# Optimization experiments

Measured on AMD Instinct MI355X. Metric: run time of the kernel, lower is better.

The kernel has to match this reference:

```python
import jax, jax.numpy as jnp
import numpy as np

N = 50000   # n_nodes
E = 800000  # n_edges (directed)
D = 64      # feature dim (in = hidden = out = 64 per source)


def setup_inputs() -> dict:
    key = jax.random.key(0)
    ks = jax.random.split(key, 16)
    s = 0.1  # init scale
    inp = {
        "x": jax.random.normal(ks[0], (N, D), jnp.float32),
        "edge_index": jax.random.randint(ks[1], (2, E), 0, N),
        # GCNConv 1
        "W1": jax.random.normal(ks[2], (D, 64), jnp.float32) * s,
        "b1": jnp.zeros((64,), jnp.float32),
        # TransformerConv (heads=1): query/key/value + root (skip) linear
        "Wq": jax.random.normal(ks[3], (64, 64), jnp.float32) * s,
        "bq": jnp.zeros((64,), jnp.float32),
        "Wk": jax.random.normal(ks[4], (64, 64), jnp.float32) * s,
        "bk": jnp.zeros((64,), jnp.float32),
        "Wv": jax.random.normal(ks[5], (64, 64), jnp.float32) * s,
        "bv": jnp.zeros((64,), jnp.float32),
        "Ws": jax.random.normal(ks[6], (64, 64), jnp.float32) * s,
        "bs": jnp.zeros((64,), jnp.float32),
        # GCNConv 2
        "W2": jax.random.normal(ks[7], (64, D), jnp.float32) * s,
        "b2": jnp.zeros((D,), jnp.float32),
    }
    return inp


def gcn_conv(x, W, b, src, dst, n):
    """PyG GCNConv: symmetric normalization with self-loops, then scatter-add."""
    xw = x @ W  # [N, F]
    loop = jnp.arange(n)
    src2 = jnp.concatenate([src, loop])
    dst2 = jnp.concatenate([dst, loop])
    deg = jax.ops.segment_sum(jnp.ones(src2.shape[0], xw.dtype), dst2, num_segments=n)
    dinv = jnp.where(deg > 0, jax.lax.rsqrt(deg), 0.0)
    norm = dinv[src2] * dinv[dst2]  # [E+N]
    out = jax.ops.segment_sum(xw[src2] * norm[:, None], dst2, num_segments=n)
    return out + b


def segment_softmax(logits, seg, n):
    m = jax.ops.segment_max(logits, seg, num_segments=n)
    e = jnp.exp(logits - m[seg])
    z = jax.ops.segment_sum(e, seg, num_segments=n)
    return e / z[seg]


def transformer_conv(x, Wq, bq, Wk, bk, Wv, bv, Ws, bs, src, dst, n):
    """PyG TransformerConv (heads=1, concat=True, root_weight=True)."""
    q = x @ Wq + bq  # [N, 64]
    k = x @ Wk + bk
    v = x @ Wv + bv
    scale = jax.lax.rsqrt(jnp.asarray(q.shape[-1], q.dtype))
    logits = jnp.sum(q[dst] * k[src], axis=-1) * scale  # [E]
    alpha = segment_softmax(logits, dst, n)
    aggr = jax.ops.segment_sum(v[src] * alpha[:, None], dst, num_segments=n)
    return aggr + x @ Ws + bs  # root/skip connection


def reference(x, edge_index, W1, b1, Wq, bq, Wk, bk, Wv, bv, Ws, bs, W2, b2):
    src, dst = edge_index[0], edge_index[1]
    n = x.shape[0]
    x1 = jax.nn.relu(gcn_conv(x, W1, b1, src, dst, n))
    x2 = transformer_conv(x1, Wq, bq, Wk, bk, Wv, bv, Ws, bs, src, dst, n)
    x3 = gcn_conv(x2, W2, b2, src, dst, n)
    return x3
```

## Files before the change

kernel.cpp:

```cpp
#include <hip/hip_runtime.h>
#include <math.h>


#define D 64
#define BKT_SHIFT 9
#define CAP 12288
#define CHUNK 4096

__device__ __forceinline__ unsigned short f2bf(float f) {
    unsigned int u = __float_as_uint(f);
    u += 0x7FFFu + ((u >> 16) & 1u);
    return (unsigned short)(u >> 16);
}
#define BF_LO(u) __uint_as_float((u) << 16)
#define BF_HI(u) __uint_as_float((u) & 0xFFFF0000u)


__global__ void init_gcursor(int* __restrict__ gcursor) {
    if (threadIdx.x < 128) gcursor[threadIdx.x] = 0;
}

__global__ __launch_bounds__(256) void binA_kernel(const int* __restrict__ src,
                                                   const int* __restrict__ dst,
                                                   int* __restrict__ gcursor,
                                                   unsigned int* __restrict__ staging,
                                                   int e, int nbkt) {
    __shared__ int cntB[128];
    __shared__ int offB[128];
    __shared__ int curB[128];
    __shared__ int gbase[128];
    __shared__ unsigned int pairs[CHUNK];
    __shared__ unsigned char bkt[CHUNK];

    int t = threadIdx.x;
    int e0 = blockIdx.x * CHUNK;
    int ecnt = min(CHUNK, e - e0);

    if (t < 128) cntB[t] = 0;
    __syncthreads();

    int myS[CHUNK / 256], myD[CHUNK / 256];
    #pragma unroll
    for (int i = 0; i < CHUNK / 256; ++i) {
        int idx = t + 256 * i;
        if (idx < ecnt) {
            myS[i] = src[e0 + idx];
            myD[i] = dst[e0 + idx];
            atomicAdd(&cntB[myD[i] >> BKT_SHIFT], 1);
        }
    }
    __syncthreads();
    if (t < 128) offB[t] = cntB[t];
    __syncthreads();
    for (int off = 1; off < 128; off <<= 1) {
        int add = (t < 128 && t >= off) ? offB[t - off] : 0;
        __syncthreads();
        if (t < 128) offB[t] += add;
        __syncthreads();
    }
    if (t < 128) {
        int excl = offB[t] - cntB[t];
        offB[t] = excl;
        curB[t] = excl;
        if (t < nbkt && cntB[t] > 0) gbase[t] = atomicAdd(&gcursor[t], cntB[t]);
    }
    __syncthreads();
    #pragma unroll
    for (int i = 0; i < CHUNK / 256; ++i) {
        int idx = t + 256 * i;
        if (idx < ecnt) {
            int b = myD[i] >> BKT_SHIFT;
            int p = atomicAdd(&curB[b], 1);
            pairs[p] = ((unsigned int)myD[i] << 16) | (unsigned int)myS[i];
            bkt[p] = (unsigned char)b;
        }
    }
    __syncthreads();
    for (int p = t; p < ecnt; p += 256) {
        int b = bkt[p];
        staging[(size_t)b * CAP + gbase[b] + (p - offB[b])] = pairs[p];
    }
}

__global__ __launch_bounds__(256) void binB_kernel(const int* __restrict__ gcursor,
                                                   const unsigned int* __restrict__ staging,
                                                   unsigned short* __restrict__ esrc,
                                                   int* __restrict__ cnt,
                                                   int* __restrict__ rowptr,
                                                   float* __restrict__ dinv,
                                                   int n, int nbkt) {
    __shared__ int bpre[128];
    __shared__ int c512[512];
    __shared__ int o512[512];
    int t = threadIdx.x;
    int b = blockIdx.x;

    if (t < 128) bpre[t] = (t < nbkt) ? gcursor[t] : 0;
    __syncthreads();
    for (int off = 1; off < 128; off <<= 1) {
        int add = (t < 128 && t >= off) ? bpre[t - off] : 0;
        __syncthreads();
        if (t < 128) bpre[t] += add;
        __syncthreads();
    }
    int base_b = (b == 0) ? 0 : bpre[b - 1];
    int cnt_b = gcursor[b];
    int lo = b << BKT_SHIFT;

    c512[t] = 0; c512[t + 256] = 0;
    __syncthreads();
    const unsigned int* st = staging + (size_t)b * CAP;
    for (int i = t; i < cnt_b; i += 256)
        atomicAdd(&c512[(int)(st[i] >> 16) - lo], 1);
    __syncthreads();
    o512[t] = c512[t]; o512[t + 256] = c512[t + 256];
    __syncthreads();
    for (int off = 1; off < 512; off <<= 1) {
        int a1 = (t >= off) ? o512[t - off] : 0;
        int a2 = o512[t + 256 - off];
        __syncthreads();
        o512[t] += a1; o512[t + 256] += a2;
        __syncthreads();
    }
    int e1 = o512[t] - c512[t];
    int e2 = o512[t + 256] - c512[t + 256];
    __syncthreads();
    o512[t] = e1; o512[t + 256] = e2;
    __syncthreads();
    for (int i = t; i < 512; i += 256) {
        int g = lo + i;
        if (g < n) {
            int c = c512[i];
            cnt[g] = c;
            rowptr[g] = base_b + o512[i];
            dinv[g] = rsqrtf((float)c + 1.0f);
        }
    }
    __syncthreads();
    for (int i = t; i < cnt_b; i += 256) {
        unsigned int pk = st[i];
        int local = (int)(pk >> 16) - lo;
        int p = atomicAdd(&o512[local], 1);
        esrc[base_b + p] = (unsigned short)(pk & 0xFFFFu);
    }
}

__global__ __launch_bounds__(256) void gemm64_bf16s(const float* __restrict__ X,
                                                    const float* __restrict__ W,
                                                    const float* __restrict__ dinv,
                                                    unsigned short* __restrict__ xs, int n) {
    __shared__ float sX[64][68];
    __shared__ float sW[64 * 64];
    int t = threadIdx.x;
    int base = blockIdx.x * 64;
    #pragma unroll
    for (int i = 0; i < 4; ++i) {
        int f = t * 4 + i * 1024;
        *(float4*)&sW[f] = *(const float4*)&W[f];
        int r = f >> 6, c = f & 63;
        int row = base + r;
        float4 xv = (row < n) ? *(const float4*)&X[(size_t)row * D + c]
                              : make_float4(0.f, 0.f, 0.f, 0.f);
        *(float4*)&sX[r][c] = xv;
    }
    __syncthreads();

    int cg = t & 15, rg = t >> 4;
    int j0 = cg * 4, r0 = rg * 4;
    float acc[4][4];
    #pragma unroll
    for (int a = 0; a < 4; ++a)
        #pragma unroll
        for (int c = 0; c < 4; ++c) acc[a][c] = 0.0f;

    #pragma unroll 4
    for (int kk = 0; kk < 64; kk += 4) {
        float4 w0 = *(const float4*)&sW[(kk + 0) * 64 + j0];
        float4 w1 = *(const float4*)&sW[(kk + 1) * 64 + j0];
        float4 w2 = *(const float4*)&sW[(kk + 2) * 64 + j0];
        float4 w3 = *(const float4*)&sW[(kk + 3) * 64 + j0];
        #pragma unroll
        for (int a = 0; a < 4; ++a) {
            float4 xv = *(const float4*)&sX[r0 + a][kk];
            acc[a][0] = fmaf(xv.x, w0.x, acc[a][0]); acc[a][1] = fmaf(xv.x, w0.y, acc[a][1]);
            acc[a][2] = fmaf(xv.x, w0.z, acc[a][2]); acc[a][3] = fmaf(xv.x, w0.w, acc[a][3]);
            acc[a][0] = fmaf(xv.y, w1.x, acc[a][0]); acc[a][1] = fmaf(xv.y, w1.y, acc[a][1]);
            acc[a][2] = fmaf(xv.y, w1.z, acc[a][2]); acc[a][3] = fmaf(xv.y, w1.w, acc[a][3]);
            acc[a][0] = fmaf(xv.z, w2.x, acc[a][0]); acc[a][1] = fmaf(xv.z, w2.y, acc[a][1]);
            acc[a][2] = fmaf(xv.z, w2.z, acc[a][2]); acc[a][3] = fmaf(xv.z, w2.w, acc[a][3]);
            acc[a][0] = fmaf(xv.w, w3.x, acc[a][0]); acc[a][1] = fmaf(xv.w, w3.y, acc[a][1]);
            acc[a][2] = fmaf(xv.w, w3.z, acc[a][2]); acc[a][3] = fmaf(xv.w, w3.w, acc[a][3]);
        }
    }

    #pragma unroll
    for (int a = 0; a < 4; ++a) {
        int row = base + r0 + a;
        if (row < n) {
            float dv = dinv[row];
            ushort4 h;
            h.x = f2bf(acc[a][0] * dv);
            h.y = f2bf(acc[a][1] * dv);
            h.z = f2bf(acc[a][2] * dv);
            h.w = f2bf(acc[a][3] * dv);
            *(ushort4*)&xs[(size_t)row * D + j0] = h;
        }
    }
}

__global__ __launch_bounds__(512) void fusedA_kernel(const unsigned short* __restrict__ xs,
                                                     const float* __restrict__ dinv,
                                                     const int* __restrict__ rowptr,
                                                     const int* __restrict__ cnt,
                                                     const unsigned short* __restrict__ esrc,
                                                     const float* __restrict__ b1,
                                                     const float* __restrict__ Wq,
                                                     const float* __restrict__ bq,
                                                     const float* __restrict__ Wk,
                                                     const float* __restrict__ bk,
                                                     const float* __restrict__ Wv,
                                                     const float* __restrict__ bv,
                                                     const float* __restrict__ Ws,
                                                     const float* __restrict__ bs,
                                                     float* __restrict__ Yq,
                                                     unsigned short* __restrict__ kv,
                                                     float* __restrict__ Ysk, int n) {
    __shared__ float sX[64][68];
    __shared__ float sW[64 * 64];
    int t = threadIdx.x;
    int base = blockIdx.x * 64;
    int local = t >> 3, sub = t & 7;
    int j0 = sub * 8;
    int node = base + local;

    {
        float a[8] = {0.f, 0.f, 0.f, 0.f, 0.f, 0.f, 0.f, 0.f};
        float4 o0 = make_float4(0.f, 0.f, 0.f, 0.f);
        float4 o1 = make_float4(0.f, 0.f, 0.f, 0.f);
        if (node < n) {
            float dd = dinv[node];
            int start = rowptr[node], deg = cnt[node];
            uint4 sr = *(const uint4*)&xs[(size_t)node * D + j0];
            a[0] += BF_LO(sr.x); a[1] += BF_HI(sr.x);
            a[2] += BF_LO(sr.y); a[3] += BF_HI(sr.y);
            a[4] += BF_LO(sr.z); a[5] += BF_HI(sr.z);
            a[6] += BF_LO(sr.w); a[7] += BF_HI(sr.w);
            int i = 0;
            for (; i + 4 <= deg; i += 4) {
                int s0 = esrc[start + i + 0];
                int s1 = esrc[start + i + 1];
                int s2 = esrc[start + i + 2];
                int s3 = esrc[start + i + 3];
                uint4 r0 = *(const uint4*)&xs[(size_t)s0 * D + j0];
                uint4 r1 = *(const uint4*)&xs[(size_t)s1 * D + j0];
                uint4 r2 = *(const uint4*)&xs[(size_t)s2 * D + j0];
                uint4 r3 = *(const uint4*)&xs[(size_t)s3 * D + j0];
                a[0] += BF_LO(r0.x) + BF_LO(r1.x) + BF_LO(r2.x) + BF_LO(r3.x);
                a[1] += BF_HI(r0.x) + BF_HI(r1.x) + BF_HI(r2.x) + BF_HI(r3.x);
                a[2] += BF_LO(r0.y) + BF_LO(r1.y) + BF_LO(r2.y) + BF_LO(r3.y);
                a[3] += BF_HI(r0.y) + BF_HI(r1.y) + BF_HI(r2.y) + BF_HI(r3.y);
                a[4] += BF_LO(r0.z) + BF_LO(r1.z) + BF_LO(r2.z) + BF_LO(r3.z);
                a[5] += BF_HI(r0.z) + BF_HI(r1.z) + BF_HI(r2.z) + BF_HI(r3.z);
                a[6] += BF_LO(r0.w) + BF_LO(r1.w) + BF_LO(r2.w) + BF_LO(r3.w);
                a[7] += BF_HI(r0.w) + BF_HI(r1.w) + BF_HI(r2.w) + BF_HI(r3.w);
            }
            for (; i < deg; ++i) {
                int s = esrc[start + i];
                uint4 r = *(const uint4*)&xs[(size_t)s * D + j0];
                a[0] += BF_LO(r.x); a[1] += BF_HI(r.x);
                a[2] += BF_LO(r.y); a[3] += BF_HI(r.y);
                a[4] += BF_LO(r.z); a[5] += BF_HI(r.z);
                a[6] += BF_LO(r.w); a[7] += BF_HI(r.w);
            }
            float4 bb0 = *(const float4*)&b1[j0];
            float4 bb1 = *(const float4*)&b1[j0 + 4];
            o0.x = fmaxf(fmaf(dd, a[0], bb0.x), 0.f);
            o0.y = fmaxf(fmaf(dd, a[1], bb0.y), 0.f);
            o0.z = fmaxf(fmaf(dd, a[2], bb0.z), 0.f);
            o0.w = fmaxf(fmaf(dd, a[3], bb0.w), 0.f);
            o1.x = fmaxf(fmaf(dd, a[4], bb1.x), 0.f);
            o1.y = fmaxf(fmaf(dd, a[5], bb1.y), 0.f);
            o1.z = fmaxf(fmaf(dd, a[6], bb1.z), 0.f);
            o1.w = fmaxf(fmaf(dd, a[7], bb1.w), 0.f);
        }
        *(float4*)&sX[local][j0] = o0;
        *(float4*)&sX[local][j0 + 4] = o1;
    }

    int cg = t & 15, rg = t >> 4;
    int gj0 = cg * 4, r0 = rg * 2;

    #pragma unroll 1
    for (int w4 = 0; w4 < 4; ++w4) {
        const float* W = (w4 == 0) ? Wq : (w4 == 1) ? Wk : (w4 == 2) ? Wv : Ws;
        const float* B = (w4 == 0) ? bq : (w4 == 1) ? bk : (w4 == 2) ? bv : bs;
        __syncthreads();
        #pragma unroll
        for (int i = 0; i < 2; ++i) {
            int f = t * 4 + i * 2048;
            *(float4*)&sW[f] = *(const float4*)&W[f];
        }
        __syncthreads();

        float acc[2][4];
        #pragma unroll
        for (int a = 0; a < 2; ++a)
            #pragma unroll
            for (int c = 0; c < 4; ++c) acc[a][c] = 0.0f;

        #pragma unroll 4
        for (int kk = 0; kk < 64; kk += 4) {
            float4 w0 = *(const float4*)&sW[(kk + 0) * 64 + gj0];
            float4 w1 = *(const float4*)&sW[(kk + 1) * 64 + gj0];
            float4 w2 = *(const float4*)&sW[(kk + 2) * 64 + gj0];
            float4 w3 = *(const float4*)&sW[(kk + 3) * 64 + gj0];
            #pragma unroll
            for (int a = 0; a < 2; ++a) {
                float4 xv = *(const float4*)&sX[r0 + a][kk];
                acc[a][0] = fmaf(xv.x, w0.x, acc[a][0]); acc[a][1] = fmaf(xv.x, w0.y, acc[a][1]);
                acc[a][2] = fmaf(xv.x, w0.z, acc[a][2]); acc[a][3] = fmaf(xv.x, w0.w, acc[a][3]);
                acc[a][0] = fmaf(xv.y, w1.x, acc[a][0]); acc[a][1] = fmaf(xv.y, w1.y, acc[a][1]);
                acc[a][2] = fmaf(xv.y, w1.z, acc[a][2]); acc[a][3] = fmaf(xv.y, w1.w, acc[a][3]);
                acc[a][0] = fmaf(xv.z, w2.x, acc[a][0]); acc[a][1] = fmaf(xv.z, w2.y, acc[a][1]);
                acc[a][2] = fmaf(xv.z, w2.z, acc[a][2]); acc[a][3] = fmaf(xv.z, w2.w, acc[a][3]);
                acc[a][0] = fmaf(xv.w, w3.x, acc[a][0]); acc[a][1] = fmaf(xv.w, w3.y, acc[a][1]);
                acc[a][2] = fmaf(xv.w, w3.z, acc[a][2]); acc[a][3] = fmaf(xv.w, w3.w, acc[a][3]);
            }
        }

        float4 bb = *(const float4*)&B[gj0];
        if (w4 == 0) {
            #pragma unroll
            for (int a = 0; a < 2; ++a) {
                int row = base + r0 + a;
                if (row < n) {
                    float4 o = make_float4((acc[a][0] + bb.x) * 0.125f,
                                           (acc[a][1] + bb.y) * 0.125f,
                                           (acc[a][2] + bb.z) * 0.125f,
                                           (acc[a][3] + bb.w) * 0.125f);
                    *(float4*)&Yq[(size_t)row * D + gj0] = o;
                }
            }
        } else if (w4 == 3) {
            #pragma unroll
            for (int a = 0; a < 2; ++a) {
                int row = base + r0 + a;
                if (row < n) {
                    float4 o = make_float4(acc[a][0] + bb.x, acc[a][1] + bb.y,
                                           acc[a][2] + bb.z, acc[a][3] + bb.w);
                    *(float4*)&Ysk[(size_t)row * D + gj0] = o;
                }
            }
        } else {
            int off = (w4 == 1) ? 0 : 64;
            #pragma unroll
            for (int a = 0; a < 2; ++a) {
                int row = base + r0 + a;
                if (row < n) {
                    ushort4 h;
                    h.x = f2bf(acc[a][0] + bb.x);
                    h.y = f2bf(acc[a][1] + bb.y);
                    h.z = f2bf(acc[a][2] + bb.z);
                    h.w = f2bf(acc[a][3] + bb.w);
                    *(ushort4*)&kv[(size_t)row * 128 + off + gj0] = h;
                }
            }
        }
    }
}

__global__ __launch_bounds__(512) void fusedB_kernel(const float* __restrict__ q,
                                                     const unsigned short* __restrict__ kv,
                                                     const float* __restrict__ skip,
                                                     const float* __restrict__ dinv,
                                                     const int* __restrict__ rowptr,
                                                     const int* __restrict__ cnt,
                                                     const unsigned short* __restrict__ esrc,
                                                     const float* __restrict__ W2,
                                                     unsigned short* __restrict__ xs2, int n) {
    __shared__ float sX[64][68];
    __shared__ float sW[64 * 64];
    int t = threadIdx.x;
    int base = blockIdx.x * 64;
    int local = t >> 3, sub = t & 7;
    int j0 = sub * 8;
    int node = base + local;

    #pragma unroll
    for (int i = 0; i < 2; ++i) {
        int f = t * 4 + i * 2048;
        *(float4*)&sW[f] = *(const float4*)&W2[f];
    }

    {
        float4 o0 = make_float4(0.f, 0.f, 0.f, 0.f);
        float4 o1 = make_float4(0.f, 0.f, 0.f, 0.f);
        if (node < n) {
            int start = rowptr[node], deg = cnt[node];
            float4 q0 = *(const float4*)&q[(size_t)node * D + j0];
            float4 q1 = *(const float4*)&q[(size_t)node * D + j0 + 4];
            float4 s0 = *(const float4*)&skip[(size_t)node * D + j0];
            float4 s1 = *(const float4*)&skip[(size_t)node * D + j0 + 4];
            float z = 0.0f;
            float a[8] = {0.f, 0.f, 0.f, 0.f, 0.f, 0.f, 0.f, 0.f};
            int i = 0;
            for (; i + 4 <= deg; i += 4) {
                int e0 = esrc[start + i + 0];
                int e1 = esrc[start + i + 1];
                int e2 = esrc[start + i + 2];
                int e3 = esrc[start + i + 3];
                const unsigned short* r0p = kv + (size_t)e0 * 128;
                const unsigned short* r1p = kv + (size_t)e1 * 128;
                const unsigned short* r2p = kv + (size_t)e2 * 128;
                const unsigned short* r3p = kv + (size_t)e3 * 128;
                uint4 k0 = *(const uint4*)&r0p[j0];
                uint4 k1 = *(const uint4*)&r1p[j0];
                uint4 k2 = *(const uint4*)&r2p[j0];
                uint4 k3 = *(const uint4*)&r3p[j0];
                uint4 v0 = *(const uint4*)&r0p[64 + j0];
                uint4 v1 = *(const uint4*)&r1p[64 + j0];
                uint4 v2 = *(const uint4*)&r2p[64 + j0];
                uint4 v3 = *(const uint4*)&r3p[64 + j0];
                float p0 = q0.x * BF_LO(k0.x) + q0.y * BF_HI(k0.x)
                         + q0.z * BF_LO(k0.y) + q0.w * BF_HI(k0.y)
                         + q1.x * BF_LO(k0.z) + q1.y * BF_HI(k0.z)
                         + q1.z * BF_LO(k0.w) + q1.w * BF_HI(k0.w);
                float p1 = q0.x * BF_LO(k1.x) + q0.y * BF_HI(k1.x)
                         + q0.z * BF_LO(k1.y) + q0.w * BF_HI(k1.y)
                         + q1.x * BF_LO(k1.z) + q1.y * BF_HI(k1.z)
                         + q1.z * BF_LO(k1.w) + q1.w * BF_HI(k1.w);
                float p2 = q0.x * BF_LO(k2.x) + q0.y * BF_HI(k2.x)
                         + q0.z * BF_LO(k2.y) + q0.w * BF_HI(k2.y)
                         + q1.x * BF_LO(k2.z) + q1.y * BF_HI(k2.z)
                         + q1.z * BF_LO(k2.w) + q1.w * BF_HI(k2.w);
                float p3 = q0.x * BF_LO(k3.x) + q0.y * BF_HI(k3.x)
                         + q0.z * BF_LO(k3.y) + q0.w * BF_HI(k3.y)
                         + q1.x * BF_LO(k3.z) + q1.y * BF_HI(k3.z)
                         + q1.z * BF_LO(k3.w) + q1.w * BF_HI(k3.w);
                #pragma unroll
                for (int off = 1; off < 8; off <<= 1) {
                    p0 += __shfl_xor(p0, off, 64);
                    p1 += __shfl_xor(p1, off, 64);
                    p2 += __shfl_xor(p2, off, 64);
                    p3 += __shfl_xor(p3, off, 64);
                }
                float w0 = __expf(p0), w1 = __expf(p1), w2 = __expf(p2), w3 = __expf(p3);
                z += (w0 + w1) + (w2 + w3);
                a[0] += w0 * BF_LO(v0.x) + w1 * BF_LO(v1.x) + w2 * BF_LO(v2.x) + w3 * BF_LO(v3.x);
                a[1] += w0 * BF_HI(v0.x) + w1 * BF_HI(v1.x) + w2 * BF_HI(v2.x) + w3 * BF_HI(v3.x);
                a[2] += w0 * BF_LO(v0.y) + w1 * BF_LO(v1.y) + w2 * BF_LO(v2.y) + w3 * BF_LO(v3.y);
                a[3] += w0 * BF_HI(v0.y) + w1 * BF_HI(v1.y) + w2 * BF_HI(v2.y) + w3 * BF_HI(v3.y);
                a[4] += w0 * BF_LO(v0.z) + w1 * BF_LO(v1.z) + w2 * BF_LO(v2.z) + w3 * BF_LO(v3.z);
                a[5] += w0 * BF_HI(v0.z) + w1 * BF_HI(v1.z) + w2 * BF_HI(v2.z) + w3 * BF_HI(v3.z);
                a[6] += w0 * BF_LO(v0.w) + w1 * BF_LO(v1.w) + w2 * BF_LO(v2.w) + w3 * BF_LO(v3.w);
                a[7] += w0 * BF_HI(v0.w) + w1 * BF_HI(v1.w) + w2 * BF_HI(v2.w) + w3 * BF_HI(v3.w);
            }
            for (; i < deg; ++i) {
                int s = esrc[start + i];
                const unsigned short* row = kv + (size_t)s * 128;
                uint4 kr = *(const uint4*)&row[j0];
                uint4 vr = *(const uint4*)&row[64 + j0];
                float p = q0.x * BF_LO(kr.x) + q0.y * BF_HI(kr.x)
                        + q0.z * BF_LO(kr.y) + q0.w * BF_HI(kr.y)
                        + q1.x * BF_LO(kr.z) + q1.y * BF_HI(kr.z)
                        + q1.z * BF_LO(kr.w) + q1.w * BF_HI(kr.w);
                #pragma unroll
                for (int off = 1; off < 8; off <<= 1) p += __shfl_xor(p, off, 64);
                float w = __expf(p);
                z += w;
                a[0] += w * BF_LO(vr.x); a[1] += w * BF_HI(vr.x);
                a[2] += w * BF_LO(vr.y); a[3] += w * BF_HI(vr.y);
                a[4] += w * BF_LO(vr.z); a[5] += w * BF_HI(vr.z);
                a[6] += w * BF_LO(vr.w); a[7] += w * BF_HI(vr.w);
            }
            if (deg > 0) {
                float inv = 1.0f / z;
                o0.x = fmaf(a[0], inv, s0.x); o0.y = fmaf(a[1], inv, s0.y);
                o0.z = fmaf(a[2], inv, s0.z); o0.w = fmaf(a[3], inv, s0.w);
                o1.x = fmaf(a[4], inv, s1.x); o1.y = fmaf(a[5], inv, s1.y);
                o1.z = fmaf(a[6], inv, s1.z); o1.w = fmaf(a[7], inv, s1.w);
            } else {
                o0 = s0; o1 = s1;
            }
        }
        *(float4*)&sX[local][j0] = o0;
        *(float4*)&sX[local][j0 + 4] = o1;
    }
    __syncthreads();

    int cg = t & 15, rg = t >> 4;
    int gj0 = cg * 4, r0 = rg * 2;
    float acc[2][4];
    #pragma unroll
    for (int a = 0; a < 2; ++a)
        #pragma unroll
        for (int c = 0; c < 4; ++c) acc[a][c] = 0.0f;

    #pragma unroll 4
    for (int kk = 0; kk < 64; kk += 4) {
        float4 w0 = *(const float4*)&sW[(kk + 0) * 64 + gj0];
        float4 w1 = *(const float4*)&sW[(kk + 1) * 64 + gj0];
        float4 w2 = *(const float4*)&sW[(kk + 2) * 64 + gj0];
        float4 w3 = *(const float4*)&sW[(kk + 3) * 64 + gj0];
        #pragma unroll
        for (int a = 0; a < 2; ++a) {
            float4 xv = *(const float4*)&sX[r0 + a][kk];
            acc[a][0] = fmaf(xv.x, w0.x, acc[a][0]); acc[a][1] = fmaf(xv.x, w0.y, acc[a][1]);
            acc[a][2] = fmaf(xv.x, w0.z, acc[a][2]); acc[a][3] = fmaf(xv.x, w0.w, acc[a][3]);
            acc[a][0] = fmaf(xv.y, w1.x, acc[a][0]); acc[a][1] = fmaf(xv.y, w1.y, acc[a][1]);
            acc[a][2] = fmaf(xv.y, w1.z, acc[a][2]); acc[a][3] = fmaf(xv.y, w1.w, acc[a][3]);
            acc[a][0] = fmaf(xv.z, w2.x, acc[a][0]); acc[a][1] = fmaf(xv.z, w2.y, acc[a][1]);
            acc[a][2] = fmaf(xv.z, w2.z, acc[a][2]); acc[a][3] = fmaf(xv.z, w2.w, acc[a][3]);
            acc[a][0] = fmaf(xv.w, w3.x, acc[a][0]); acc[a][1] = fmaf(xv.w, w3.y, acc[a][1]);
            acc[a][2] = fmaf(xv.w, w3.z, acc[a][2]); acc[a][3] = fmaf(xv.w, w3.w, acc[a][3]);
        }
    }

    #pragma unroll
    for (int a = 0; a < 2; ++a) {
        int row = base + r0 + a;
        if (row < n) {
            float dv = dinv[row];
            ushort4 h;
            h.x = f2bf(acc[a][0] * dv);
            h.y = f2bf(acc[a][1] * dv);
            h.z = f2bf(acc[a][2] * dv);
            h.w = f2bf(acc[a][3] * dv);
            *(ushort4*)&xs2[(size_t)row * D + gj0] = h;
        }
    }
}

__global__ __launch_bounds__(256) void gcn_gather_kernel(const unsigned short* __restrict__ xs,
                                                         const float* __restrict__ dinv,
                                                         const int* __restrict__ rowptr,
                                                         const int* __restrict__ cnt,
                                                         const unsigned short* __restrict__ esrc,
                                                         const float* __restrict__ bias,
                                                         float* __restrict__ out,
                                                         int n, int relu) {
    int node = (blockIdx.x * blockDim.x + threadIdx.x) >> 6;
    if (node >= n) return;
    int lane = threadIdx.x & 63;
    int grp = lane >> 3;
    int sub = lane & 7;
    int j0 = sub * 8;

    int start = rowptr[node], deg = cnt[node];

    float a[8] = {0.f, 0.f, 0.f, 0.f, 0.f, 0.f, 0.f, 0.f};
    int i = grp;
    int sNext = (i < deg) ? esrc[start + i] : 0;
    for (; i < deg; i += 8) {
        int s = sNext;
        int in = i + 8;
        if (in < deg) sNext = esrc[start + in];
        uint4 r = *(const uint4*)&xs[(size_t)s * D + j0];
        a[0] += BF_LO(r.x); a[1] += BF_HI(r.x);
        a[2] += BF_LO(r.y); a[3] += BF_HI(r.y);
        a[4] += BF_LO(r.z); a[5] += BF_HI(r.z);
        a[6] += BF_LO(r.w); a[7] += BF_HI(r.w);
    }
    #pragma unroll
    for (int off = 8; off < 64; off <<= 1) {
        #pragma unroll
        for (int c = 0; c < 8; ++c) a[c] += __shfl_xor(a[c], off, 64);
    }

    if (grp == 0) {
        float dd = dinv[node];
        uint4 sr = *(const uint4*)&xs[(size_t)node * D + j0];
        a[0] += BF_LO(sr.x); a[1] += BF_HI(sr.x);
        a[2] += BF_LO(sr.y); a[3] += BF_HI(sr.y);
        a[4] += BF_LO(sr.z); a[5] += BF_HI(sr.z);
        a[6] += BF_LO(sr.w); a[7] += BF_HI(sr.w);
        float4 b0 = *(const float4*)&bias[j0];
        float4 b1 = *(const float4*)&bias[j0 + 4];
        float o[8];
        o[0] = fmaf(dd, a[0], b0.x); o[1] = fmaf(dd, a[1], b0.y);
        o[2] = fmaf(dd, a[2], b0.z); o[3] = fmaf(dd, a[3], b0.w);
        o[4] = fmaf(dd, a[4], b1.x); o[5] = fmaf(dd, a[5], b1.y);
        o[6] = fmaf(dd, a[6], b1.z); o[7] = fmaf(dd, a[7], b1.w);
        if (relu) {
            #pragma unroll
            for (int c = 0; c < 8; ++c) o[c] = fmaxf(o[c], 0.f);
        }
        *(float4*)&out[(size_t)node * D + j0] = make_float4(o[0], o[1], o[2], o[3]);
        *(float4*)&out[(size_t)node * D + j0 + 4] = make_float4(o[4], o[5], o[6], o[7]);
    }
}


extern "C" void kernel_launch(void* const* d_in, const int* in_sizes, int n_in,
                              void* d_out, int out_size, void* d_ws, size_t ws_size,
                              hipStream_t stream) {
    const float* x  = (const float*)d_in[0];
    const int*   ei = (const int*)d_in[1];
    const float* W1 = (const float*)d_in[2];
    const float* b1 = (const float*)d_in[3];
    const float* Wq = (const float*)d_in[4];
    const float* bq = (const float*)d_in[5];
    const float* Wk = (const float*)d_in[6];
    const float* bk = (const float*)d_in[7];
    const float* Wv = (const float*)d_in[8];
    const float* bv = (const float*)d_in[9];
    const float* Ws = (const float*)d_in[10];
    const float* bs = (const float*)d_in[11];
    const float* W2 = (const float*)d_in[12];
    const float* b2 = (const float*)d_in[13];
    float* out = (float*)d_out;

    const int n = in_sizes[0] / D;
    const int e = in_sizes[1] / 2;
    const int* src = ei;
    const int* dst = ei + e;
    const int n64 = n * D;
    const int nbkt = (n + (1 << BKT_SHIFT) - 1) >> BKT_SHIFT;

    char* w = (char*)d_ws;
    auto carve = [&](size_t bytes) {
        char* p = w;
        w += (bytes + 255) & ~(size_t)255;
        return p;
    };
    int* gcursor            = (int*)carve(128 * 4);
    unsigned int* staging   = (unsigned int*)carve((size_t)nbkt * CAP * 4);
    unsigned short* esrc    = (unsigned short*)carve((size_t)e * 2);
    int* cnt                = (int*)carve((size_t)n * 4);
    int* rowptr             = (int*)carve((size_t)n * 4);
    float* dinv             = (float*)carve((size_t)n * 4);
    float* bufQ             = (float*)carve((size_t)n64 * 4);
    unsigned short* xs      = (unsigned short*)carve((size_t)n64 * 2);
    unsigned short* kv      = (unsigned short*)carve((size_t)n64 * 4);

    const int nb_binA = (e + CHUNK - 1) / CHUNK;
    const int nb_nw   = (n + 3) / 4;
    const int nb_g    = (n + 63) / 64;

    init_gcursor<<<1, 128, 0, stream>>>(gcursor);
    binA_kernel<<<nb_binA, 256, 0, stream>>>(src, dst, gcursor, staging, e, nbkt);
    binB_kernel<<<nbkt, 256, 0, stream>>>(gcursor, staging, esrc, cnt, rowptr, dinv, n, nbkt);

    gemm64_bf16s<<<nb_g, 256, 0, stream>>>(x, W1, dinv, xs, n);

    fusedA_kernel<<<nb_g, 512, 0, stream>>>(xs, dinv, rowptr, cnt, esrc, b1,
                                            Wq, bq, Wk, bk, Wv, bv, Ws, bs,
                                            bufQ, kv, out, n);

    fusedB_kernel<<<nb_g, 512, 0, stream>>>(bufQ, kv, out, dinv,
                                            rowptr, cnt, esrc, W2, xs, n);

    gcn_gather_kernel<<<nb_nw, 256, 0, stream>>>(xs, dinv, rowptr, cnt, esrc,
                                                 b2, out, n, 0);
}
```

Before: 252.2 us.

## Sort nodes by in-degree and process them through a permutation for load balance

Result: slower. 509.6 us (+102.1%).

```diff
diff --git a/kernel.cpp b/kernel.cpp
--- a/kernel.cpp
+++ b/kernel.cpp
@@ -17,7 +17,7 @@
 
 
 __global__ void init_gcursor(int* __restrict__ gcursor) {
-    if (threadIdx.x < 128) gcursor[threadIdx.x] = 0;
+    if (threadIdx.x < 192) gcursor[threadIdx.x] = 0;
 }
 
 __global__ __launch_bounds__(256) void binA_kernel(const int* __restrict__ src,
@@ -88,6 +88,7 @@
                                                    int* __restrict__ cnt,
                                                    int* __restrict__ rowptr,
                                                    float* __restrict__ dinv,
+                                                   int* __restrict__ deghist,
                                                    int n, int nbkt) {
     __shared__ int bpre[128];
     __shared__ int c512[512];
@@ -134,6 +135,7 @@
             cnt[g] = c;
             rowptr[g] = base_b + o512[i];
             dinv[g] = rsqrtf((float)c + 1.0f);
+            atomicAdd(&deghist[63 - min(c, 63)], 1);
         }
     }
     __syncthreads();
@@ -142,6 +144,27 @@
         int local = (int)(pk >> 16) - lo;
         int p = atomicAdd(&o512[local], 1);
         esrc[base_b + p] = (unsigned short)(pk & 0xFFFFu);
+    }
+}
+
+__global__ void degscan_kernel(int* __restrict__ deghist) {
+    if (threadIdx.x == 0) {
+        int run = 0;
+        for (int i = 0; i < 64; ++i) {
+            int c = deghist[i];
+            deghist[i] = run;
+            run += c;
+        }
+    }
+}
+
+__global__ void degscatter_kernel(const int* __restrict__ cnt, int* __restrict__ degbase,
+                                  int* __restrict__ perm, int n) {
+    int i = blockIdx.x * blockDim.x + threadIdx.x;
+    if (i < n) {
+        int bin = 63 - min(cnt[i], 63);
+        int pos = atomicAdd(&degbase[bin], 1);
+        perm[pos] = i;
     }
 }
 
@@ -213,6 +236,7 @@
                                                      const int* __restrict__ rowptr,
                                                      const int* __restrict__ cnt,
                                                      const unsigned short* __restrict__ esrc,
+                                                     const int* __restrict__ perm,
                                                      const float* __restrict__ b1,
                                                      const float* __restrict__ Wq,
                                                      const float* __restrict__ bq,
@@ -227,17 +251,20 @@
                                                      float* __restrict__ Ysk, int n) {
     __shared__ float sX[64][68];
     __shared__ float sW[64 * 64];
+    __shared__ int sPerm[64];
     int t = threadIdx.x;
     int base = blockIdx.x * 64;
     int local = t >> 3, sub = t & 7;
     int j0 = sub * 8;
-    int node = base + local;
+
+    if (t < 64) sPerm[t] = (base + t < n) ? perm[base + t] : -1;
 
     {
+        int node = (base + local < n) ? perm[base + local] : -1;
         float a[8] = {0.f, 0.f, 0.f, 0.f, 0.f, 0.f, 0.f, 0.f};
         float4 o0 = make_float4(0.f, 0.f, 0.f, 0.f);
         float4 o1 = make_float4(0.f, 0.f, 0.f, 0.f);
-        if (node < n) {
+        if (node >= 0) {
             float dd = dinv[node];
             int start = rowptr[node], deg = cnt[node];
             uint4 sr = *(const uint4*)&xs[(size_t)node * D + j0];
@@ -332,37 +359,37 @@
         if (w4 == 0) {
             #pragma unroll
             for (int a = 0; a < 2; ++a) {
-                int row = base + r0 + a;
-                if (row < n) {
+                int pr = sPerm[r0 + a];
+                if (pr >= 0) {
                     float4 o = make_float4((acc[a][0] + bb.x) * 0.125f,
                                            (acc[a][1] + bb.y) * 0.125f,
                                            (acc[a][2] + bb.z) * 0.125f,
                                            (acc[a][3] + bb.w) * 0.125f);
-                    *(float4*)&Yq[(size_t)row * D + gj0] = o;
+                    *(float4*)&Yq[(size_t)pr * D + gj0] = o;
                 }
             }
         } else if (w4 == 3) {
             #pragma unroll
             for (int a = 0; a < 2; ++a) {
-                int row = base + r0 + a;
-                if (row < n) {
+                int pr = sPerm[r0 + a];
+                if (pr >= 0) {
                     float4 o = make_float4(acc[a][0] + bb.x, acc[a][1] + bb.y,
                                            acc[a][2] + bb.z, acc[a][3] + bb.w);
-                    *(float4*)&Ysk[(size_t)row * D + gj0] = o;
+                    *(float4*)&Ysk[(size_t)pr * D + gj0] = o;
                 }
             }
         } else {
             int off = (w4 == 1) ? 0 : 64;
             #pragma unroll
             for (int a = 0; a < 2; ++a) {
-                int row = base + r0 + a;
-                if (row < n) {
+                int pr = sPerm[r0 + a];
+                if (pr >= 0) {
                     ushort4 h;
                     h.x = f2bf(acc[a][0] + bb.x);
                     h.y = f2bf(acc[a][1] + bb.y);
                     h.z = f2bf(acc[a][2] + bb.z);
                     h.w = f2bf(acc[a][3] + bb.w);
-                    *(ushort4*)&kv[(size_t)row * 128 + off + gj0] = h;
+                    *(ushort4*)&kv[(size_t)pr * 128 + off + gj0] = h;
                 }
             }
         }
@@ -376,15 +403,18 @@
                                                      const int* __restrict__ rowptr,
                                                      const int* __restrict__ cnt,
                                                      const unsigned short* __restrict__ esrc,
+                                                     const int* __restrict__ perm,
                                                      const float* __restrict__ W2,
                                                      unsigned short* __restrict__ xs2, int n) {
     __shared__ float sX[64][68];
     __shared__ float sW[64 * 64];
+    __shared__ int sPerm[64];
     int t = threadIdx.x;
     int base = blockIdx.x * 64;
     int local = t >> 3, sub = t & 7;
     int j0 = sub * 8;
-    int node = base + local;
+
+    if (t < 64) sPerm[t] = (base + t < n) ? perm[base + t] : -1;
 
     #pragma unroll
     for (int i = 0; i < 2; ++i) {
@@ -393,9 +423,10 @@
     }
 
     {
+        int node = (base + local < n) ? perm[base + local] : -1;
         float4 o0 = make_float4(0.f, 0.f, 0.f, 0.f);
         float4 o1 = make_float4(0.f, 0.f, 0.f, 0.f);
-        if (node < n) {
+        if (node >= 0) {
             int start = rowptr[node], deg = cnt[node];
             float4 q0 = *(const float4*)&q[(size_t)node * D + j0];
             float4 q1 = *(const float4*)&q[(size_t)node * D + j0 + 4];
@@ -518,15 +549,15 @@
 
     #pragma unroll
     for (int a = 0; a < 2; ++a) {
-        int row = base + r0 + a;
-        if (row < n) {
-            float dv = dinv[row];
+        int pr = sPerm[r0 + a];
+        if (pr >= 0) {
+            float dv = dinv[pr];
             ushort4 h;
             h.x = f2bf(acc[a][0] * dv);
             h.y = f2bf(acc[a][1] * dv);
             h.z = f2bf(acc[a][2] * dv);
             h.w = f2bf(acc[a][3] * dv);
-            *(ushort4*)&xs2[(size_t)row * D + gj0] = h;
+            *(ushort4*)&xs2[(size_t)pr * D + gj0] = h;
         }
     }
 }
@@ -536,11 +567,13 @@
                                                          const int* __restrict__ rowptr,
                                                          const int* __restrict__ cnt,
                                                          const unsigned short* __restrict__ esrc,
+                                                         const int* __restrict__ perm,
                                                          const float* __restrict__ bias,
                                                          float* __restrict__ out,
                                                          int n, int relu) {
-    int node = (blockIdx.x * blockDim.x + threadIdx.x) >> 6;
-    if (node >= n) return;
+    int slot = (blockIdx.x * blockDim.x + threadIdx.x) >> 6;
+    if (slot >= n) return;
+    int node = perm[slot];
     int lane = threadIdx.x & 63;
     int grp = lane >> 3;
     int sub = lane & 7;
@@ -623,33 +656,39 @@
         w += (bytes + 255) & ~(size_t)255;
         return p;
     };
-    int* gcursor            = (int*)carve(128 * 4);
+    int* gcursor            = (int*)carve(192 * 4);
+    int* deghist            = gcursor + 128;
     unsigned int* staging   = (unsigned int*)carve((size_t)nbkt * CAP * 4);
     unsigned short* esrc    = (unsigned short*)carve((size_t)e * 2);
     int* cnt                = (int*)carve((size_t)n * 4);
     int* rowptr             = (int*)carve((size_t)n * 4);
     float* dinv             = (float*)carve((size_t)n * 4);
+    int* perm               = (int*)carve((size_t)n * 4);
     float* bufQ             = (float*)carve((size_t)n64 * 4);
     unsigned short* xs      = (unsigned short*)carve((size_t)n64 * 2);
     unsigned short* kv      = (unsigned short*)carve((size_t)n64 * 4);
 
     const int nb_binA = (e + CHUNK - 1) / CHUNK;
+    const int nb_n    = (n + 255) / 256;
     const int nb_nw   = (n + 3) / 4;
     const int nb_g    = (n + 63) / 64;
 
-    init_gcursor<<<1, 128, 0, stream>>>(gcursor);
+    init_gcursor<<<1, 256, 0, stream>>>(gcursor);
     binA_kernel<<<nb_binA, 256, 0, stream>>>(src, dst, gcursor, staging, e, nbkt);
-    binB_kernel<<<nbkt, 256, 0, stream>>>(gcursor, staging, esrc, cnt, rowptr, dinv, n, nbkt);
+    binB_kernel<<<nbkt, 256, 0, stream>>>(gcursor, staging, esrc, cnt, rowptr, dinv,
+                                          deghist, n, nbkt);
+    degscan_kernel<<<1, 64, 0, stream>>>(deghist);
+    degscatter_kernel<<<nb_n, 256, 0, stream>>>(cnt, deghist, perm, n);
 
     gemm64_bf16s<<<nb_g, 256, 0, stream>>>(x, W1, dinv, xs, n);
 
-    fusedA_kernel<<<nb_g, 512, 0, stream>>>(xs, dinv, rowptr, cnt, esrc, b1,
+    fusedA_kernel<<<nb_g, 512, 0, stream>>>(xs, dinv, rowptr, cnt, esrc, perm, b1,
                                             Wq, bq, Wk, bk, Wv, bv, Ws, bs,
                                             bufQ, kv, out, n);
 
     fusedB_kernel<<<nb_g, 512, 0, stream>>>(bufQ, kv, out, dinv,
-                                            rowptr, cnt, esrc, W2, xs, n);
-
-    gcn_gather_kernel<<<nb_nw, 256, 0, stream>>>(xs, dinv, rowptr, cnt, esrc,
+                                            rowptr, cnt, esrc, perm, W2, xs, n);
+
+    gcn_gather_kernel<<<nb_nw, 256, 0, stream>>>(xs, dinv, rowptr, cnt, esrc, perm,
                                                  b2, out, n, 0);
 }
```
